# Optimization experiments

Measured on AMD Instinct MI355X. Metric: run time of the kernel, lower is better.

The kernel has to match this reference:

```python
import jax, jax.numpy as jnp
import numpy as np

Q, B, DM, H, HD, MEM = 1024, 4, 1024, 16, 64, 512
KLEN = MEM + Q
MLP = 4096
SCALE = 1.0 / np.sqrt(HD)
EPS = 1e-5


def _layer_norm(x, g, b):
    m = jnp.mean(x, axis=-1, keepdims=True)
    var = jnp.mean(jnp.square(x - m), axis=-1, keepdims=True)
    return (x - m) * jax.lax.rsqrt(var + EPS) * g + b


def _rel_shift(x):
    # x: [qlen, klen, batch, heads] -> Transformer-XL relative shift
    q, k, b, h = x.shape
    x = jnp.pad(x, ((0, 0), (1, 0), (0, 0), (0, 0)))  # [q, k+1, b, h]
    x = x.reshape(k + 1, q, b, h)[1:]                  # drop first row
    return x.reshape(q, k, b, h)


def setup_inputs() -> dict:
    key = jax.random.key(0)
    ks = jax.random.split(key, 16)
    s = 0.02
    inputs = jax.random.normal(ks[0], (Q, B, DM), jnp.float32)
    r = jax.random.normal(ks[1], (KLEN, DM), jnp.float32)
    u = jax.random.normal(ks[2], (H, HD), jnp.float32) * s
    v = jax.random.normal(ks[3], (H, HD), jnp.float32) * s
    mem = jax.random.normal(ks[4], (MEM, B, DM), jnp.float32)
    # causal mask with memory: query i may attend to keys j <= i + MEM
    i = jnp.arange(Q)[:, None]
    j = jnp.arange(KLEN)[None, :]
    attn_mask = j > (i + MEM)  # True = masked
    W_qkv = jax.random.normal(ks[5], (DM, 3 * H * HD), jnp.float32) * s
    W_r = jax.random.normal(ks[6], (DM, H * HD), jnp.float32) * s
    W_o = jax.random.normal(ks[7], (H * HD, DM), jnp.float32) * s
    ln1_g = jnp.ones((DM,), jnp.float32)
    ln1_b = jnp.zeros((DM,), jnp.float32)
    ln2_g = jnp.ones((DM,), jnp.float32)
    ln2_b = jnp.zeros((DM,), jnp.float32)
    W1 = jax.random.normal(ks[8], (DM, MLP), jnp.float32) * s
    b1 = jnp.zeros((MLP,), jnp.float32)
    W2 = jax.random.normal(ks[9], (MLP, DM), jnp.float32) * s
    b2 = jnp.zeros((DM,), jnp.float32)
    return {"inputs": inputs, "r": r, "u": u, "v": v, "mem": mem,
            "attn_mask": attn_mask, "W_qkv": W_qkv, "W_r": W_r, "W_o": W_o,
            "ln1_g": ln1_g, "ln1_b": ln1_b, "ln2_g": ln2_g, "ln2_b": ln2_b,
            "W1": W1, "b1": b1, "W2": W2, "b2": b2}


def reference(inputs, r, u, v, mem, attn_mask, W_qkv, W_r, W_o,
              ln1_g, ln1_b, ln2_g, ln2_b, W1, b1, W2, b2):
    qlen = inputs.shape[0]
    cat = jnp.concatenate([mem, inputs], axis=0)      # [klen, B, DM]
    klen = cat.shape[0]
    qkv = cat @ W_qkv                                  # [klen, B, 3*H*HD]
    q_h, k_h, v_h = jnp.split(qkv, 3, axis=-1)
    q_h = q_h[-qlen:].reshape(qlen, -1, H, HD)         # [q, B, H, HD]
    k_h = k_h.reshape(klen, -1, H, HD)                 # [k, B, H, HD]
    v_h = v_h.reshape(klen, -1, H, HD)
    r_h = (r @ W_r).reshape(klen, H, HD)               # [k, H, HD]
    # content score (AC) + position score (BD, rel-shifted)
    AC = jnp.einsum('ibhd,jbhd->ijbh', q_h + u, k_h)
    BD = _rel_shift(jnp.einsum('ibhd,jhd->ijbh', q_h + v, r_h))
    score = (AC + BD) * SCALE                          # [q, k, B, H]
    score = jnp.where(attn_mask[:, :, None, None], jnp.float32(-1e30), score)
    attn = jax.nn.softmax(score, axis=1)
    ctx = jnp.einsum('ijbh,jbhd->ibhd', attn, v_h).reshape(qlen, -1, H * HD)
    y = ctx @ W_o                                      # [q, B, DM]
    x = _layer_norm(inputs + y, ln1_g, ln1_b)
    h = jax.nn.relu(x @ W1 + b1)
    y2 = h @ W2 + b2
    return _layer_norm(x + y2, ln2_g, ln2_b)
```

## Files before the change

### kernel.cpp

```cpp
#include <hip/hip_runtime.h>
#include <hip/hip_bf16.h>

typedef __hip_bfloat16 bf16;
typedef _Float16 f16;
typedef __attribute__((ext_vector_type(8))) short short8;
typedef __attribute__((ext_vector_type(4))) float f32x4;
typedef __attribute__((ext_vector_type(8))) _Float16 f16x8;
typedef __attribute__((ext_vector_type(4))) _Float16 f16x4;

#define Q_LEN 1024
#define B_SZ 4
#define DM 1024
#define H_CNT 16
#define HD 64
#define MEM_LEN 512
#define KLEN 1536
#define MLP 4096

__device__ __forceinline__ void store_c(float* p, float v) { *p = v; }
__device__ __forceinline__ void store_c(bf16* p, float v) { *p = __float2bfloat16(v); }
__device__ __forceinline__ void store_c(f16* p, float v) { *p = (f16)v; }

__device__ __forceinline__ float b2f(short s) {
  union { unsigned u; float f; } x;
  x.u = ((unsigned)(unsigned short)s) << 16;
  return x.f;
}
__device__ __forceinline__ short f2b(float f) {
  union { float f; unsigned u; } x;
  x.f = f;
  unsigned r = x.u + 0x7fff + ((x.u >> 16) & 1);
  return (short)(r >> 16);
}

__device__ __forceinline__ void gload16(const void* g, void* l) {
  __builtin_amdgcn_global_load_lds(
      (__attribute__((address_space(1))) unsigned int*)(g),
      (__attribute__((address_space(3))) unsigned int*)(l), 16, 0, 0);
}

__global__ __launch_bounds__(256) void convh_kernel(
    const float* __restrict__ X, f16* __restrict__ Y, int n4) {
  const int i = blockIdx.x * 256 + threadIdx.x;
  if (i < n4) {
    f32x4 v = *(const f32x4*)&X[(size_t)i * 4];
    f16x4 h;
#pragma unroll
    for (int j = 0; j < 4; ++j) h[j] = (f16)v[j];
    *(f16x4*)&Y[(size_t)i * 4] = h;
  }
}

__global__ __launch_bounds__(256) void convT_kernel(
    const float* __restrict__ W, f16* __restrict__ WT, int K, int N) {
  __shared__ float tile[64][65];
  const int tid = threadIdx.x;
  const int k0 = blockIdx.y * 64, n0 = blockIdx.x * 64;
  const int tn = tid & 63, tk4 = tid >> 6;
#pragma unroll
  for (int p = 0; p < 16; ++p) {
    const int kk = tk4 + p * 4;
    tile[kk][tn] = W[(size_t)(k0 + kk) * N + n0 + tn];
  }
  __syncthreads();
#pragma unroll
  for (int p = 0; p < 16; ++p) {
    const int nn = tk4 + p * 4;
    WT[(size_t)(n0 + nn) * K + k0 + tn] = (f16)tile[tn][nn];
  }
}

template <typename TC>
__global__ __launch_bounds__(256, 3) void hgemm_kernel(
    const f16* __restrict__ A, const f16* __restrict__ BT, TC* __restrict__ C,
    int M, int N, int K, const float* __restrict__ bias, int relu,
    const f16* __restrict__ Aalt, TC* __restrict__ Calt, int split) {
  __shared__ __align__(16) f16 sA[3][128 * 32];
  __shared__ __align__(16) f16 sB[3][128 * 32];
  const int tid = threadIdx.x;
  const int w = tid >> 6, lane = tid & 63;
  const int quad = lane >> 4, m16 = lane & 15;
  const int wr = w >> 1, wc = w & 1;
  const int gx = gridDim.x;
  const int nwg = gx * gridDim.y;
  const int lin = blockIdx.y * gx + blockIdx.x;
  const int cpx = nwg >> 3;
  const int swz = (lin & 7) * cpx + (lin >> 3);
  const int bx = swz % gx, by = swz / gx;
  const int col0 = bx * 128;
  int r0 = by * 128;
  const f16* Ause = A;
  TC* Cuse = C;
  if (r0 >= split) { Ause = Aalt; Cuse = Calt; r0 -= split; }

  const int strow = tid >> 2;
  const int schunk = tid & 3;
  const int sw = schunk ^ ((strow >> 1) & 3);
  const f16* gA0 = Ause + (size_t)(r0 + strow) * K + sw * 8;
  const f16* gB0 = BT + (size_t)(col0 + strow) * K + sw * 8;
  f16* ldsA0 = &sA[0][0] + (size_t)w * 512;
  f16* ldsB0 = &sB[0][0] + (size_t)w * 512;

  const int qs = quad ^ ((m16 >> 1) & 3);
  int aoff[4], boff[4];
#pragma unroll
  for (int i = 0; i < 4; ++i) {
    aoff[i] = (wr * 64 + i * 16 + m16) * 32 + qs * 8;
    boff[i] = (wc * 64 + i * 16 + m16) * 32 + qs * 8;
  }

  const int nkt = K >> 5;
  f32x4 acc[4][4] = {};

  auto stage = [&](int buf, int t) {
    const int k0 = t << 5;
    const size_t bufo = (size_t)buf * 4096;
    gload16(gA0 + k0, ldsA0 + bufo);
    gload16(gA0 + (size_t)64 * K + k0, ldsA0 + bufo + 2048);
    gload16(gB0 + k0, ldsB0 + bufo);
    gload16(gB0 + (size_t)64 * K + k0, ldsB0 + bufo + 2048);
  };

  stage(0, 0);
  stage(1, 1);
  int cur = 0;
  for (int t = 0; t < nkt; ++t) {
    if (t + 1 < nkt) {
      asm volatile("s_waitcnt vmcnt(4)" ::: "memory");
    } else {
      asm volatile("s_waitcnt vmcnt(0)" ::: "memory");
    }
    __builtin_amdgcn_s_barrier();
    if (t + 2 < nkt) {
      int nb = cur + 2;
      if (nb >= 3) nb -= 3;
      stage(nb, t + 2);
    }
    f16x8 af[4], bfr[4];
#pragma unroll
    for (int i = 0; i < 4; ++i) af[i] = *(const f16x8*)&sA[cur][aoff[i]];
#pragma unroll
    for (int i = 0; i < 4; ++i) bfr[i] = *(const f16x8*)&sB[cur][boff[i]];
    __builtin_amdgcn_s_setprio(1);
#pragma unroll
    for (int mi = 0; mi < 4; ++mi)
#pragma unroll
      for (int ni = 0; ni < 4; ++ni)
        acc[mi][ni] = __builtin_amdgcn_mfma_f32_16x16x32_f16(
            af[mi], bfr[ni], acc[mi][ni], 0, 0, 0);
    __builtin_amdgcn_s_setprio(0);
    cur = (cur + 1 == 3) ? 0 : cur + 1;
  }

#pragma unroll
  for (int mi = 0; mi < 4; ++mi) {
    const int row = r0 + wr * 64 + mi * 16 + quad * 4;
#pragma unroll
    for (int ni = 0; ni < 4; ++ni) {
      const int col = col0 + wc * 64 + ni * 16 + m16;
      const float bv = bias ? bias[col] : 0.f;
#pragma unroll
      for (int rg = 0; rg < 4; ++rg) {
        float vv = acc[mi][ni][rg] + bv;
        if (relu) vv = vv > 0.f ? vv : 0.f;
        store_c(&Cuse[(size_t)(row + rg) * N + col], vv);
      }
    }
  }
}

__global__ __launch_bounds__(256, 4) void fattn_kernel(
    const bf16* __restrict__ qkvp,
    const bf16* __restrict__ rhp,
    const float* __restrict__ u, const float* __restrict__ v,
    float* __restrict__ ctx) {
  const int lin = blockIdx.x;
  const int p = lin & 63;
  const int b = p & 3, h = p >> 2;
  const int i0 = (15 - (lin >> 6)) * 64;
  const int tid = threadIdx.x;
  const int w = tid >> 6, lane = tid & 63;
  const int quad = lane >> 4, m16 = lane & 15;

  __shared__ short sVt[64 * 40];
  __shared__ short sR[96 * 72];
  __shared__ short sProb[64 * 40];

  const short* qkv = (const short*)qkvp;
  const short* rh  = (const short*)rhp;

  short8 aQu0, aQu1, aQv0, aQv1;
  {
    const size_t qro = ((size_t)(512 + i0 + w * 16 + m16) * 4 + b) * 3072 + h * 64 + quad * 8;
    short8 qa = *(const short8*)&qkv[qro];
    short8 qb = *(const short8*)&qkv[qro + 32];
    const float* up = u + h * 64 + quad * 8;
    const float* vp = v + h * 64 + quad * 8;
#pragma unroll
    for (int j = 0; j < 8; ++j) {
      const float qaf = b2f(qa[j]), qbf = b2f(qb[j]);
      aQu0[j] = f2b(qaf + up[j]);
      aQu1[j] = f2b(qbf + up[j + 32]);
      aQv0[j] = f2b(qaf + vp[j]);
      aQv1[j] = f2b(qbf + vp[j + 32]);
    }
  }

  const int st_row = tid >> 3, st_d0 = (tid & 7) * 8;
  const int vj = lane & 31, vd0 = w * 16 + (lane >> 5) * 8;

#pragma unroll
  for (int p_ = 0; p_ < 3; ++p_) {
    int t = 960 - i0 + p_ * 32 + st_row;
    t = t > 1535 ? 1535 : t;
    *(short8*)&sR[(p_ * 32 + st_row) * 72 + st_d0] =
        *(const short8*)&rh[(size_t)t * 1024 + h * 64 + st_d0];
  }
  {
    short8 v8 = *(const short8*)&qkv[((size_t)vj * 4 + b) * 3072 + 2048 + h * 64 + vd0];
#pragma unroll
    for (int q = 0; q < 8; ++q) sVt[(vd0 + q) * 40 + vj] = v8[q];
  }
  short8 rKf[4];
#pragma unroll
  for (int n0i = 0; n0i < 2; ++n0i) {
    const size_t kro = ((size_t)(n0i * 16 + m16) * 4 + b) * 3072 + 1024 + h * 64 + quad * 8;
    rKf[n0i * 2] = *(const short8*)&qkv[kro];
    rKf[n0i * 2 + 1] = *(const short8*)&qkv[kro + 32];
  }

  short8 ones;
#pragma unroll
  for (int q = 0; q < 8; ++q) ones[q] = (short)0x3F80;

  f32x4 O[4] = {};
  f32x4 L = {};
  float m = -1e30f;
  int bk = 0;
  int tnext = 1056 - i0;

  const int n_kt = ((i0 + 575) >> 5) + 1;
  for (int kt = 0; kt < n_kt; ++kt) {
    const int j0 = kt * 32;
    const bool pf = (kt + 1 < n_kt);
    __syncthreads();

    short8 nV, nR;
    if (pf) {
      nV = *(const short8*)&qkv[((size_t)(j0 + 32 + vj) * 4 + b) * 3072 + 2048 + h * 64 + vd0];
      int t = tnext + st_row;
      t = t > 1535 ? 1535 : t;
      nR = *(const short8*)&rh[(size_t)t * 1024 + h * 64 + st_d0];
    }

    f32x4 ac[2];
#pragma unroll
    for (int n0i = 0; n0i < 2; ++n0i) {
      f32x4 a = {};
      a = __builtin_amdgcn_mfma_f32_16x16x32_bf16(aQu0, rKf[n0i * 2], a, 0, 0, 0);
      a = __builtin_amdgcn_mfma_f32_16x16x32_bf16(aQu1, rKf[n0i * 2 + 1], a, 0, 0, 0);
      ac[n0i] = a;
    }
    if (pf) {
#pragma unroll
      for (int n0i = 0; n0i < 2; ++n0i) {
        const size_t kro = ((size_t)(j0 + 32 + n0i * 16 + m16) * 4 + b) * 3072 + 1024 + h * 64 + quad * 8;
        rKf[n0i * 2] = *(const short8*)&qkv[kro];
        rKf[n0i * 2 + 1] = *(const short8*)&qkv[kro + 32];
      }
    }

    f32x4 pb[3];
#pragma unroll
    for (int pt = 0; pt < 3; ++pt) {
      const int p0 = 48 - 16 * w + 16 * pt;
      int pr = bk + p0;
      if (pr >= 96) pr -= 96;
      int row = pr + m16;
      if (row >= 96) row -= 96;
      const short8 bR0 = *(const short8*)&sR[row * 72 + quad * 8];
      const short8 bR1 = *(const short8*)&sR[row * 72 + 32 + quad * 8];
      f32x4 pf_ = {};
      pf_ = __builtin_amdgcn_mfma_f32_16x16x32_bf16(aQv0, bR0, pf_, 0, 0, 0);
      pf_ = __builtin_amdgcn_mfma_f32_16x16x32_bf16(aQv1, bR1, pf_, 0, 0, 0);
      pb[pt] = pf_;
    }

    float S0[4], S1[4];
    float mxl = -1e30f;
#pragma unroll
    for (int rg = 0; rg < 4; ++rg) {
      const int rloc = quad * 4 + rg;
      const int irow = i0 + w * 16 + rloc;
      const int c0 = m16 - rloc + 15;
      const int src = (lane & 48) | (c0 & 15);
      const float t0 = __shfl(pb[0][rg], src);
      const float t1 = __shfl(pb[1][rg], src);
      const float t2 = __shfl(pb[2][rg], src);
      const float p0v = (c0 < 16) ? t0 : t1;
      const float p1v = (c0 < 16) ? t1 : t2;
      float s0 = (ac[0][rg] + p0v) * 0.125f;
      float s1 = (ac[1][rg] + p1v) * 0.125f;
      if (j0 + m16 > irow + 512) s0 = -1e30f;
      if (j0 + 16 + m16 > irow + 512) s1 = -1e30f;
      S0[rg] = s0;
      S1[rg] = s1;
      mxl = fmaxf(mxl, fmaxf(s0, s1));
    }
    mxl = fmaxf(mxl, __shfl_xor(mxl, 1));
    mxl = fmaxf(mxl, __shfl_xor(mxl, 2));
    mxl = fmaxf(mxl, __shfl_xor(mxl, 4));
    mxl = fmaxf(mxl, __shfl_xor(mxl, 8));
    mxl = fmaxf(mxl, __shfl_xor(mxl, 16));
    mxl = fmaxf(mxl, __shfl_xor(mxl, 32));
    const float mnew = fmaxf(m, mxl);
    const float al = __expf(m - mnew);
    m = mnew;
#pragma unroll
    for (int rg = 0; rg < 4; ++rg) {
      const int rloc = quad * 4 + rg;
      sProb[(w * 16 + rloc) * 40 + m16] = f2b(__expf(S0[rg] - mnew));
      sProb[(w * 16 + rloc) * 40 + 16 + m16] = f2b(__expf(S1[rg] - mnew));
    }
#pragma unroll
    for (int d0i = 0; d0i < 4; ++d0i)
#pragma unroll
      for (int rg = 0; rg < 4; ++rg) O[d0i][rg] *= al;
#pragma unroll
    for (int rg = 0; rg < 4; ++rg) L[rg] *= al;

    const short8 aP = *(const short8*)&sProb[(w * 16 + m16) * 40 + quad * 8];
    L = __builtin_amdgcn_mfma_f32_16x16x32_bf16(aP, ones, L, 0, 0, 0);
#pragma unroll
    for (int d0i = 0; d0i < 4; ++d0i) {
      const short8 bV = *(const short8*)&sVt[(d0i * 16 + m16) * 40 + quad * 8];
      O[d0i] = __builtin_amdgcn_mfma_f32_16x16x32_bf16(aP, bV, O[d0i], 0, 0, 0);
    }

    __syncthreads();
    if (pf) {
#pragma unroll
      for (int q = 0; q < 8; ++q) sVt[(vd0 + q) * 40 + vj] = nV[q];
      *(short8*)&sR[(bk + st_row) * 72 + st_d0] = nR;
    }
    bk += 32;
    if (bk >= 96) bk = 0;
    tnext += 32;
  }

#pragma unroll
  for (int d0i = 0; d0i < 4; ++d0i) {
#pragma unroll
    for (int rg = 0; rg < 4; ++rg) {
      const int irow = i0 + w * 16 + quad * 4 + rg;
      ctx[((size_t)irow * 4 + b) * 1024 + h * 64 + d0i * 16 + m16] = O[d0i][rg] / L[rg];
    }
  }
}

__global__ __launch_bounds__(256) void ln1_kernel(
    const bf16* __restrict__ y, const float* __restrict__ inp,
    const float* __restrict__ g, const float* __restrict__ beta,
    float* __restrict__ xo, f16* __restrict__ xh) {
  const int r = blockIdx.x, tid = threadIdx.x;
  __shared__ float red[256];
  float t[4];
  float s = 0.f;
#pragma unroll
  for (int q = 0; q < 4; ++q) {
    int c = tid + q * 256;
    t[q] = __bfloat162float(y[(size_t)r * DM + c]) + inp[(size_t)r * DM + c];
    s += t[q];
  }
  red[tid] = s;
  __syncthreads();
  for (int st = 128; st > 0; st >>= 1) {
    if (tid < st) red[tid] += red[tid + st];
    __syncthreads();
  }
  const float mean = red[0] * (1.f / DM);
  __syncthreads();
  float vs = 0.f;
#pragma unroll
  for (int q = 0; q < 4; ++q) {
    float d0 = t[q] - mean;
    vs += d0 * d0;
  }
  red[tid] = vs;
  __syncthreads();
  for (int st = 128; st > 0; st >>= 1) {
    if (tid < st) red[tid] += red[tid + st];
    __syncthreads();
  }
  const float rstd = rsqrtf(red[0] * (1.f / DM) + 1e-5f);
#pragma unroll
  for (int q = 0; q < 4; ++q) {
    int c = tid + q * 256;
    const float val = (t[q] - mean) * rstd * g[c] + beta[c];
    xo[(size_t)r * DM + c] = val;
    xh[(size_t)r * DM + c] = (f16)val;
  }
}

__global__ __launch_bounds__(256) void ln2_kernel(
    const float* __restrict__ x, const bf16* __restrict__ y2,
    const float* __restrict__ b2, const float* __restrict__ g,
    const float* __restrict__ beta, float* __restrict__ out) {
  const int r = blockIdx.x, tid = threadIdx.x;
  __shared__ float red[256];
  float t[4];
  float s = 0.f;
#pragma unroll
  for (int q = 0; q < 4; ++q) {
    int c = tid + q * 256;
    t[q] = x[(size_t)r * DM + c] + __bfloat162float(y2[(size_t)r * DM + c]) + b2[c];
    s += t[q];
  }
  red[tid] = s;
  __syncthreads();
  for (int st = 128; st > 0; st >>= 1) {
    if (tid < st) red[tid] += red[tid + st];
    __syncthreads();
  }
  const float mean = red[0] * (1.f / DM);
  __syncthreads();
  float vs = 0.f;
#pragma unroll
  for (int q = 0; q < 4; ++q) {
    float d0 = t[q] - mean;
    vs += d0 * d0;
  }
  red[tid] = vs;
  __syncthreads();
  for (int st = 128; st > 0; st >>= 1) {
    if (tid < st) red[tid] += red[tid + st];
    __syncthreads();
  }
  const float rstd = rsqrtf(red[0] * (1.f / DM) + 1e-5f);
#pragma unroll
  for (int q = 0; q < 4; ++q) {
    int c = tid + q * 256;
    out[(size_t)r * DM + c] = (t[q] - mean) * rstd * g[c] + beta[c];
  }
}

extern "C" void kernel_launch(void* const* d_in, const int* in_sizes, int n_in,
                              void* d_out, int out_size, void* d_ws, size_t ws_size,
                              hipStream_t stream) {
  const int o = (n_in >= 17) ? 1 : 0;
  const float* inputs = (const float*)d_in[0];
  const float* r      = (const float*)d_in[1];
  const float* u      = (const float*)d_in[2];
  const float* v      = (const float*)d_in[3];
  const float* memp   = (const float*)d_in[4];
  const float* W_qkv  = (const float*)d_in[5 + o];
  const float* W_r    = (const float*)d_in[6 + o];
  const float* W_o    = (const float*)d_in[7 + o];
  const float* ln1_g  = (const float*)d_in[8 + o];
  const float* ln1_b  = (const float*)d_in[9 + o];
  const float* ln2_g  = (const float*)d_in[10 + o];
  const float* ln2_b  = (const float*)d_in[11 + o];
  const float* W1     = (const float*)d_in[12 + o];
  const float* b1     = (const float*)d_in[13 + o];
  const float* W2     = (const float*)d_in[14 + o];
  const float* b2     = (const float*)d_in[15 + o];

  char* ws = (char*)d_ws;
  f16*  WqkvT = (f16*)(ws);
  f16*  r16   = (f16*)(ws + 6291456);
  f16*  WrT   = (f16*)(ws + 9437184);
  bf16* qkv   = (bf16*)(ws + 11534336);
  bf16* rh    = (bf16*)(ws + 49283072);
  f16*  cat_h = (f16*)d_out;
  float* ctx  = (float*)d_out;
  f16*  ctx_h = (f16*)(ws);
  f16*  WoT   = (f16*)(ws + 8388608);
  bf16* y     = (bf16*)(ws + 10485760);
  float* x    = (float*)(ws + 18874368);
  f16*  x_h   = (f16*)(ws + 35651584);
  f16*  W1T   = (f16*)(ws + 44040192);
  f16*  h_lo  = (f16*)d_out;
  f16*  h_hi  = (f16*)(ws);
  f16*  W2T   = (f16*)(ws + 35651584);
  bf16* y2    = (bf16*)(ws + 44040192);

  dim3 blk(256);
  const int BIG = 1 << 30;

  convh_kernel<<<dim3(2048), blk, 0, stream>>>(memp, cat_h, 524288);
  convh_kernel<<<dim3(4096), blk, 0, stream>>>(inputs, cat_h + (size_t)2048 * 1024, 1048576);
  convh_kernel<<<dim3(1536), blk, 0, stream>>>(r, r16, 393216);
  convT_kernel<<<dim3(48, 16), blk, 0, stream>>>(W_qkv, WqkvT, 1024, 3072);
  convT_kernel<<<dim3(16, 16), blk, 0, stream>>>(W_r, WrT, 1024, 1024);
  hgemm_kernel<bf16><<<dim3(24, 48), blk, 0, stream>>>(
      cat_h, WqkvT, qkv, 6144, 3072, 1024, nullptr, 0, nullptr, nullptr, BIG);
  hgemm_kernel<bf16><<<dim3(8, 12), blk, 0, stream>>>(
      r16, WrT, rh, 1536, 1024, 1024, nullptr, 0, nullptr, nullptr, BIG);
  fattn_kernel<<<dim3(1024), blk, 0, stream>>>(qkv, rh, u, v, ctx);

  convh_kernel<<<dim3(4096), blk, 0, stream>>>(ctx, ctx_h, 1048576);
  convT_kernel<<<dim3(16, 16), blk, 0, stream>>>(W_o, WoT, 1024, 1024);
  hgemm_kernel<bf16><<<dim3(8, 32), blk, 0, stream>>>(
      ctx_h, WoT, y, 4096, 1024, 1024, nullptr, 0, nullptr, nullptr, BIG);
  ln1_kernel<<<dim3(4096), blk, 0, stream>>>(y, inputs, ln1_g, ln1_b, x, x_h);
  convT_kernel<<<dim3(64, 16), blk, 0, stream>>>(W1, W1T, 1024, 4096);
  hgemm_kernel<f16><<<dim3(32, 32), blk, 0, stream>>>(
      x_h, W1T, h_lo, 4096, 4096, 1024, b1, 1,
      x_h + (size_t)2048 * 1024, h_hi, 2048);
  convT_kernel<<<dim3(16, 64), blk, 0, stream>>>(W2, W2T, 4096, 1024);
  hgemm_kernel<bf16><<<dim3(8, 32), blk, 0, stream>>>(
      h_lo, W2T, y2, 4096, 1024, 4096, nullptr, 0,
      h_hi, y2 + (size_t)2048 * 1024, 2048);
  ln2_kernel<<<dim3(4096), blk, 0, stream>>>(x, y2, b2, ln2_g, ln2_b, (float*)d_out);
}
```

Before: 529.0 us.

## Split-K the Wo and W2 GEMMs and emit f16 context directly from attention

Adds a two-way split-K mode to the GEMM kernel and uses it for the output projection and the second MLP GEMM. Each grid launches twice as many workgroups that write partial sums to separate f16 buffers, which the layer-norm kernels then add, so these N=1024 GEMMs fill more of the GPU. The attention kernel now writes f16 context directly, which removes a separate conversion pass. LN1 no longer writes an fp32 copy of x, and LN2 reads the f16 residual instead. This lowers precision on the residual and on the partial sums.

```diff
diff --git a/kernel.cpp b/kernel.cpp
--- a/kernel.cpp
+++ b/kernel.cpp
@@ -72,9 +72,10 @@
 
 template <typename TC>
 __global__ __launch_bounds__(256, 3) void hgemm_kernel(
-    const f16* __restrict__ A, const f16* __restrict__ BT, TC* __restrict__ C,
-    int M, int N, int K, const float* __restrict__ bias, int relu,
-    const f16* __restrict__ Aalt, TC* __restrict__ Calt, int split) {
+    const f16* __restrict__ A, const f16* __restrict__ BT, TC* C,
+    int N, int K, const float* __restrict__ bias, int relu,
+    const f16* __restrict__ Aalt, TC* Calt, int split,
+    TC* Cb, TC* Cbalt, int ksplit) {
   __shared__ __align__(16) f16 sA[3][128 * 32];
   __shared__ __align__(16) f16 sB[3][128 * 32];
   const int tid = threadIdx.x;
@@ -86,7 +87,14 @@
   const int lin = blockIdx.y * gx + blockIdx.x;
   const int cpx = nwg >> 3;
   const int swz = (lin & 7) * cpx + (lin >> 3);
-  const int bx = swz % gx, by = swz / gx;
+  const int bx = swz % gx;
+  int by = swz / gx;
+  int koff = 0, Kloc = K;
+  if (ksplit == 2) {
+    const int mh = gridDim.y >> 1;
+    if (by >= mh) { by -= mh; koff = K >> 1; C = Cb; Calt = Cbalt; }
+    Kloc = K >> 1;
+  }
   const int col0 = bx * 128;
   int r0 = by * 128;
   const f16* Ause = A;
@@ -96,8 +104,8 @@
   const int strow = tid >> 2;
   const int schunk = tid & 3;
   const int sw = schunk ^ ((strow >> 1) & 3);
-  const f16* gA0 = Ause + (size_t)(r0 + strow) * K + sw * 8;
-  const f16* gB0 = BT + (size_t)(col0 + strow) * K + sw * 8;
+  const f16* gA0 = Ause + (size_t)(r0 + strow) * K + koff + sw * 8;
+  const f16* gB0 = BT + (size_t)(col0 + strow) * K + koff + sw * 8;
   f16* ldsA0 = &sA[0][0] + (size_t)w * 512;
   f16* ldsB0 = &sB[0][0] + (size_t)w * 512;
 
@@ -109,7 +117,7 @@
     boff[i] = (wc * 64 + i * 16 + m16) * 32 + qs * 8;
   }
 
-  const int nkt = K >> 5;
+  const int nkt = Kloc >> 5;
   f32x4 acc[4][4] = {};
 
   auto stage = [&](int buf, int t) {
@@ -173,7 +181,7 @@
     const bf16* __restrict__ qkvp,
     const bf16* __restrict__ rhp,
     const float* __restrict__ u, const float* __restrict__ v,
-    float* __restrict__ ctx) {
+    f16* __restrict__ ctxh) {
   const int lin = blockIdx.x;
   const int p = lin & 63;
   const int b = p & 3, h = p >> 2;
@@ -353,15 +361,16 @@
 #pragma unroll
     for (int rg = 0; rg < 4; ++rg) {
       const int irow = i0 + w * 16 + quad * 4 + rg;
-      ctx[((size_t)irow * 4 + b) * 1024 + h * 64 + d0i * 16 + m16] = O[d0i][rg] / L[rg];
+      ctxh[((size_t)irow * 4 + b) * 1024 + h * 64 + d0i * 16 + m16] =
+          (f16)(O[d0i][rg] / L[rg]);
     }
   }
 }
 
 __global__ __launch_bounds__(256) void ln1_kernel(
-    const bf16* __restrict__ y, const float* __restrict__ inp,
-    const float* __restrict__ g, const float* __restrict__ beta,
-    float* __restrict__ xo, f16* __restrict__ xh) {
+    const f16* __restrict__ ya, const f16* __restrict__ yb,
+    const float* __restrict__ inp, const float* __restrict__ g,
+    const float* __restrict__ beta, f16* __restrict__ xh) {
   const int r = blockIdx.x, tid = threadIdx.x;
   __shared__ float red[256];
   float t[4];
@@ -369,7 +378,8 @@
 #pragma unroll
   for (int q = 0; q < 4; ++q) {
     int c = tid + q * 256;
-    t[q] = __bfloat162float(y[(size_t)r * DM + c]) + inp[(size_t)r * DM + c];
+    t[q] = (float)ya[(size_t)r * DM + c] + (float)yb[(size_t)r * DM + c] +
+           inp[(size_t)r * DM + c];
     s += t[q];
   }
   red[tid] = s;
@@ -397,15 +407,15 @@
   for (int q = 0; q < 4; ++q) {
     int c = tid + q * 256;
     const float val = (t[q] - mean) * rstd * g[c] + beta[c];
-    xo[(size_t)r * DM + c] = val;
     xh[(size_t)r * DM + c] = (f16)val;
   }
 }
 
 __global__ __launch_bounds__(256) void ln2_kernel(
-    const float* __restrict__ x, const bf16* __restrict__ y2,
-    const float* __restrict__ b2, const float* __restrict__ g,
-    const float* __restrict__ beta, float* __restrict__ out) {
+    const f16* __restrict__ xh, const f16* __restrict__ y2a,
+    const f16* __restrict__ y2b, const float* __restrict__ b2,
+    const float* __restrict__ g, const float* __restrict__ beta,
+    float* __restrict__ out) {
   const int r = blockIdx.x, tid = threadIdx.x;
   __shared__ float red[256];
   float t[4];
@@ -413,7 +423,8 @@
 #pragma unroll
   for (int q = 0; q < 4; ++q) {
     int c = tid + q * 256;
-    t[q] = x[(size_t)r * DM + c] + __bfloat162float(y2[(size_t)r * DM + c]) + b2[c];
+    t[q] = (float)xh[(size_t)r * DM + c] + (float)y2a[(size_t)r * DM + c] +
+           (float)y2b[(size_t)r * DM + c] + b2[c];
     s += t[q];
   }
   red[tid] = s;
@@ -472,17 +483,17 @@
   bf16* qkv   = (bf16*)(ws + 11534336);
   bf16* rh    = (bf16*)(ws + 49283072);
   f16*  cat_h = (f16*)d_out;
-  float* ctx  = (float*)d_out;
   f16*  ctx_h = (f16*)(ws);
   f16*  WoT   = (f16*)(ws + 8388608);
-  bf16* y     = (bf16*)(ws + 10485760);
-  float* x    = (float*)(ws + 18874368);
-  f16*  x_h   = (f16*)(ws + 35651584);
-  f16*  W1T   = (f16*)(ws + 44040192);
+  f16*  ya    = (f16*)(ws + 10485760);
+  f16*  yb    = (f16*)(ws + 18874368);
+  f16*  x_h   = (f16*)(ws + 27262976);
+  f16*  W1T   = (f16*)(ws + 35651584);
+  f16*  h_hi  = (f16*)(ws);
   f16*  h_lo  = (f16*)d_out;
-  f16*  h_hi  = (f16*)(ws);
-  f16*  W2T   = (f16*)(ws + 35651584);
-  bf16* y2    = (bf16*)(ws + 44040192);
+  f16*  W2T   = (f16*)(ws + 44040192);
+  f16*  y2a   = (f16*)(ws + 18874368);
+  f16*  y2b   = (f16*)(ws + 35651584);
 
   dim3 blk(256);
   const int BIG = 1 << 30;
@@ -493,23 +504,27 @@
   convT_kernel<<<dim3(48, 16), blk, 0, stream>>>(W_qkv, WqkvT, 1024, 3072);
   convT_kernel<<<dim3(16, 16), blk, 0, stream>>>(W_r, WrT, 1024, 1024);
   hgemm_kernel<bf16><<<dim3(24, 48), blk, 0, stream>>>(
-      cat_h, WqkvT, qkv, 6144, 3072, 1024, nullptr, 0, nullptr, nullptr, BIG);
+      cat_h, WqkvT, qkv, 3072, 1024, nullptr, 0,
+      nullptr, nullptr, BIG, nullptr, nullptr, 1);
   hgemm_kernel<bf16><<<dim3(8, 12), blk, 0, stream>>>(
-      r16, WrT, rh, 1536, 1024, 1024, nullptr, 0, nullptr, nullptr, BIG);
-  fattn_kernel<<<dim3(1024), blk, 0, stream>>>(qkv, rh, u, v, ctx);
-
-  convh_kernel<<<dim3(4096), blk, 0, stream>>>(ctx, ctx_h, 1048576);
+      r16, WrT, rh, 1024, 1024, nullptr, 0,
+      nullptr, nullptr, BIG, nullptr, nullptr, 1);
+  fattn_kernel<<<dim3(1024), blk, 0, stream>>>(qkv, rh, u, v, ctx_h);
+
   convT_kernel<<<dim3(16, 16), blk, 0, stream>>>(W_o, WoT, 1024, 1024);
-  hgemm_kernel<bf16><<<dim3(8, 32), blk, 0, stream>>>(
-      ctx_h, WoT, y, 4096, 1024, 1024, nullptr, 0, nullptr, nullptr, BIG);
-  ln1_kernel<<<dim3(4096), blk, 0, stream>>>(y, inputs, ln1_g, ln1_b, x, x_h);
+  hgemm_kernel<f16><<<dim3(8, 64), blk, 0, stream>>>(
+      ctx_h, WoT, ya, 1024, 1024, nullptr, 0,
+      nullptr, nullptr, BIG, yb, nullptr, 2);
+  ln1_kernel<<<dim3(4096), blk, 0, stream>>>(ya, yb, inputs, ln1_g, ln1_b, x_h);
   convT_kernel<<<dim3(64, 16), blk, 0, stream>>>(W1, W1T, 1024, 4096);
   hgemm_kernel<f16><<<dim3(32, 32), blk, 0, stream>>>(
-      x_h, W1T, h_lo, 4096, 4096, 1024, b1, 1,
-      x_h + (size_t)2048 * 1024, h_hi, 2048);
+      x_h, W1T, h_lo, 4096, 1024, b1, 1,
+      x_h + (size_t)2048 * 1024, h_hi, 2048, nullptr, nullptr, 1);
   convT_kernel<<<dim3(16, 64), blk, 0, stream>>>(W2, W2T, 4096, 1024);
-  hgemm_kernel<bf16><<<dim3(8, 32), blk, 0, stream>>>(
-      h_lo, W2T, y2, 4096, 1024, 4096, nullptr, 0,
-      h_hi, y2 + (size_t)2048 * 1024, 2048);
-  ln2_kernel<<<dim3(4096), blk, 0, stream>>>(x, y2, b2, ln2_g, ln2_b, (float*)d_out);
-}
+  hgemm_kernel<f16><<<dim3(8, 64), blk, 0, stream>>>(
+      h_lo, W2T, y2a, 1024, 4096, nullptr, 0,
+      h_hi, y2a + (size_t)2048 * 1024, 2048,
+      y2b, y2b + (size_t)2048 * 1024, 2);
+  ln2_kernel<<<dim3(4096), blk, 0, stream>>>(x_h, y2a, y2b, b2, ln2_g, ln2_b,
+                                             (float*)d_out);
+}
```

Measured after the change: 483.4 us. 1.09x faster.
